# Kernel optimization log

Hardware: AMD Instinct MI355X
Metric: run time of the kernel (lower is better)

The kernel has to match this reference:

```python
import jax, jax.numpy as jnp
import numpy as np

DIM, H, DH = 3072, 24, 128
MLP = int(DIM * 4.0)
EPS = 1e-6


def setup_inputs() -> dict:
    key = jax.random.key(0)
    ks = jax.random.split(key, 8)
    B, L = 2, 4096
    s = 0.02
    return {
        "hidden_states": jax.random.normal(ks[0], (B, L, DIM), jnp.float32),
        "temb": jax.random.normal(ks[1], (B, DIM), jnp.float32),
        "rope": jax.random.normal(ks[2], (L, DH // 2, 4), jnp.float32),
        "w_lin": jax.random.normal(ks[3], (DIM, 3 * DIM), jnp.float32) * s,
        "b_lin": jnp.zeros((3 * DIM,), jnp.float32),
        "w1": jax.random.normal(ks[4], (DIM, 3 * DIM + MLP), jnp.float32) * s,
        "b1": jnp.zeros((3 * DIM + MLP,), jnp.float32),
        "w2": jax.random.normal(ks[5], (DIM + MLP, DIM), jnp.float32) * s,
        "b2": jnp.zeros((DIM,), jnp.float32),
        "q_scale": jnp.ones((DH,), jnp.float32),
        "k_scale": jnp.ones((DH,), jnp.float32),
    }


def _rms(x, scale):
    return x * jax.lax.rsqrt(jnp.mean(x * x, axis=-1, keepdims=True) + EPS) * scale


def _rope(x, fr):
    # x: [B,H,L,DH]; fr: [L, DH//2, 2, 2]
    B, Hn, L, D = x.shape
    x_ = x.reshape(B, Hn, L, D // 2, 1, 2)
    out = fr[..., 0] * x_[..., 0] + fr[..., 1] * x_[..., 1]  # [B,H,L,D//2,2]
    return out.reshape(B, Hn, L, D)


def reference(hidden_states, temb, rope, w_lin, b_lin, w1, b1, w2, b2, q_scale, k_scale):
    B, L, _ = hidden_states.shape
    residual = hidden_states
    # AdaLayerNormZeroSingle
    emb = jax.nn.silu(temb) @ w_lin + b_lin  # [B, 3*DIM]
    shift, scale, gate = jnp.split(emb[:, None, :], 3, axis=-1)
    mu = jnp.mean(hidden_states, axis=-1, keepdims=True)
    var = jnp.mean(jnp.square(hidden_states - mu), axis=-1, keepdims=True)
    x = (hidden_states - mu) * jax.lax.rsqrt(var + EPS)
    x = x * (1 + scale) + shift
    # fused QKV + MLP projection
    proj = x @ w1 + b1
    qkv, mlp = proj[..., : 3 * DIM], proj[..., 3 * DIM :]
    qkv = qkv.reshape(B, L, 3, H, DH).transpose(2, 0, 3, 1, 4)  # [3,B,H,L,DH]
    q, k, v = qkv[0], qkv[1], qkv[2]
    q = _rms(q, q_scale)
    k = _rms(k, k_scale)
    fr = rope.reshape(L, DH // 2, 2, 2)
    q = _rope(q, fr)
    k = _rope(k, fr)
    # heads are MERGED before attention (faithful to source)
    q = q.transpose(0, 2, 1, 3).reshape(B, L, H * DH)
    k = k.transpose(0, 2, 1, 3).reshape(B, L, H * DH)
    v = v.transpose(0, 2, 1, 3).reshape(B, L, H * DH)
    attn = jax.nn.softmax(jnp.einsum("bqd,bkd->bqk", q, k) * (DH ** -0.5), axis=-1)
    attn_out = jnp.einsum("bqk,bkd->bqd", attn, v)
    h = jnp.concatenate([attn_out, jax.nn.gelu(mlp)], axis=-1) @ w2 + b2
    return residual + gate * h
```

## Files before the change

kernel.cpp:

```cpp
#include <hip/hip_runtime.h>
#include <hip/hip_fp16.h>

typedef _Float16 half_t;
typedef __attribute__((ext_vector_type(8))) _Float16 f16x8;
typedef __attribute__((ext_vector_type(4))) float f32x4;

#define DIM   3072
#define NH    24
#define DH    128
#define MLP_D 12288
#define LSEQ  4096
#define BATCH 2
#define NROWS 8192
#define N1    21504
#define QKV_N 9216
#define CAT_N 15360

__device__ __forceinline__ void gload16(const void* g, void* l) {
  __builtin_amdgcn_global_load_lds((const __attribute__((address_space(1))) void*)g,
                                   (__attribute__((address_space(3))) void*)l, 16, 0, 0);
}

__device__ __forceinline__ float gelu_tanh(float x) {
  float u = 0.7978845608028654f * (x + 0.044715f * x * x * x);
  float t = 1.f - 2.f / (__expf(2.f * u) + 1.f);
  return 0.5f * x * (1.f + t);
}

struct EpiParams {
  const float* bias;
  float* outF; int ldoF;
  half_t* o1; int ldo1;
  half_t* o2; int ldo2;
  const float* resid;
  const float* gate;
  float scale;
};

template<int EPI>
__global__ __launch_bounds__(512, 2) void gemm256(
    const half_t* __restrict__ A, int lda,
    const half_t* __restrict__ B, int ldb,
    int nbx, int nper, size_t strA, size_t strB, size_t strO,
    int nsplit, int K, EpiParams ep)
{
  __shared__ __align__(16) char lds[131072];
  const int t = threadIdx.x, lane = t & 63, wid = t >> 6;

  const int nwg = gridDim.x;
  const int wg = blockIdx.x;
  const int id = (wg & 7) * (nwg >> 3) + (wg >> 3);
  const int bz = id / nper;
  const int rid = id - bz * nper;
  const int panel = 8 * nbx;
  const int bm = (rid / panel) * 8 + (rid % 8);
  const int bn = (rid % panel) / 8;
  const int brow = bm * 256, bcol = bn * 256;
  const int wr = wid >> 2, wc = wid & 3;
  A += bz * strA;
  B += bz * strB;

  f32x4 acc[8][4];
#pragma unroll
  for (int m = 0; m < 8; ++m)
#pragma unroll
    for (int n = 0; n < 4; ++n) acc[m][n] = (f32x4){0.f, 0.f, 0.f, 0.f};

  const int scol = (((lane & 3) ^ ((lane >> 3) & 3)) * 8);
  const half_t* pA = A + (size_t)(brow + wid * 32 + (lane >> 2)) * lda + scol;
  const half_t* pB = B + (size_t)(bcol + wid * 32 + (lane >> 2)) * ldb + scol;
  const int wrow = wid * 2048;
  const int NT = K >> 6;

  const int pc = (((lane >> 4) ^ ((lane >> 1) & 3)) << 4);
  const int aoff = (wr * 128 + (lane & 15)) * 64 + pc;
  const int boff = 32768 + (wc * 64 + (lane & 15)) * 64 + pc;

  f16x8 af[2][4], bf[2][4];

#define STAGE_A(bb, kh, tk) {                                               \
    gload16(pA + (size_t)(tk) * 64 + (kh) * 32,                             \
            (bb) + (kh) * 16384 + wrow);                                    \
    gload16(pA + (size_t)(tk) * 64 + (kh) * 32 + (size_t)16 * lda,          \
            (bb) + (kh) * 16384 + wrow + 1024); }
#define STAGE_B(bb, kh, tk) {                                               \
    gload16(pB + (size_t)(tk) * 64 + (kh) * 32,                             \
            (bb) + 32768 + (kh) * 16384 + wrow);                            \
    gload16(pB + (size_t)(tk) * 64 + (kh) * 32 + (size_t)16 * ldb,          \
            (bb) + 32768 + (kh) * 16384 + wrow + 1024); }

#define MFMA_Q(accoff, ab, bb2)                                             \
    _Pragma("unroll")                                                       \
    for (int mi = 0; mi < 4; ++mi)                                          \
      _Pragma("unroll")                                                     \
      for (int nj = 0; nj < 4; ++nj)                                        \
        acc[(accoff) + mi][nj] = __builtin_amdgcn_mfma_f32_16x16x32_f16(    \
            af[ab][mi], bf[bb2][nj], acc[(accoff) + mi][nj], 0, 0, 0);

  {
    char* b0 = lds;
    char* b1 = lds + 65536;
    STAGE_B(b0, 0, 0); STAGE_A(b0, 0, 0); STAGE_B(b0, 1, 0); STAGE_A(b0, 1, 0);
    STAGE_B(b1, 0, 1); STAGE_A(b1, 0, 1); STAGE_B(b1, 1, 1); STAGE_A(b1, 1, 1);
    asm volatile("s_waitcnt vmcnt(8)" ::: "memory");
    __builtin_amdgcn_s_barrier();
#pragma unroll
    for (int mi = 0; mi < 4; ++mi) af[0][mi] = *(const f16x8*)(lds + aoff + mi * 1024);
#pragma unroll
    for (int nj = 0; nj < 4; ++nj) bf[0][nj] = *(const f16x8*)(lds + boff + nj * 1024);
    __builtin_amdgcn_s_barrier();
  }

  for (int tt = 0; tt < NT; ++tt) {
    char* cb = lds + (size_t)(tt & 1) * 65536;
    char* nb = lds + (size_t)((tt & 1) ^ 1) * 65536;

    __builtin_amdgcn_s_setprio(1);
    MFMA_Q(0, 0, 0)
    __builtin_amdgcn_s_setprio(0);
#pragma unroll
    for (int mi = 0; mi < 4; ++mi) af[1][mi] = *(const f16x8*)(cb + aoff + 4096 + mi * 1024);
    if (tt + 2 < NT) STAGE_B(cb, 0, tt + 2);
    __builtin_amdgcn_s_barrier();

    __builtin_amdgcn_s_setprio(1);
    MFMA_Q(4, 1, 0)
    __builtin_amdgcn_s_setprio(0);
#pragma unroll
    for (int mi = 0; mi < 4; ++mi) af[0][mi] = *(const f16x8*)(cb + aoff + 16384 + mi * 1024);
#pragma unroll
    for (int nj = 0; nj < 4; ++nj) bf[1][nj] = *(const f16x8*)(cb + boff + 16384 + nj * 1024);
    if (tt + 2 < NT) STAGE_A(cb, 0, tt + 2);
    __builtin_amdgcn_s_barrier();

    __builtin_amdgcn_s_setprio(1);
    MFMA_Q(0, 0, 1)
    __builtin_amdgcn_s_setprio(0);
#pragma unroll
    for (int mi = 0; mi < 4; ++mi) af[1][mi] = *(const f16x8*)(cb + aoff + 16384 + 4096 + mi * 1024);
    if (tt + 2 < NT) STAGE_B(cb, 1, tt + 2);
    if (tt + 2 < NT) asm volatile("s_waitcnt vmcnt(6)" ::: "memory");
    else             asm volatile("s_waitcnt vmcnt(0)" ::: "memory");
    __builtin_amdgcn_s_barrier();

    __builtin_amdgcn_s_setprio(1);
    MFMA_Q(4, 1, 1)
    __builtin_amdgcn_s_setprio(0);
    if (tt + 1 < NT) {
#pragma unroll
      for (int mi = 0; mi < 4; ++mi) af[0][mi] = *(const f16x8*)(nb + aoff + mi * 1024);
#pragma unroll
      for (int nj = 0; nj < 4; ++nj) bf[0][nj] = *(const f16x8*)(nb + boff + nj * 1024);
    }
    if (tt + 2 < NT) STAGE_A(cb, 1, tt + 2);
    __builtin_amdgcn_s_barrier();
  }
#undef STAGE_A
#undef STAGE_B
#undef MFMA_Q

  half_t* o1 = ep.o1;
  half_t* o2 = ep.o2;
  if (EPI == 1) o1 += (size_t)bz * strO;
  if (EPI == 2) o2 += (size_t)bz * strO;
  const int laneR = lane & 15;
  const int colb = bcol + wc * 64;
  const int rowb = brow + wr * 128 + (lane >> 4) * 4;
#pragma unroll
  for (int mi = 0; mi < 8; ++mi) {
#pragma unroll
    for (int nj = 0; nj < 4; ++nj) {
      int col = colb + nj * 16 + laneR;
#pragma unroll
      for (int j = 0; j < 4; ++j) {
        int row = rowb + mi * 16 + j;
        float v = acc[mi][nj][j];
        if (EPI == 0) {
          v += ep.bias[col];
          if (col < nsplit) {
            o1[(size_t)row * ep.ldo1 + col] = (half_t)v;
          } else {
            o2[(size_t)row * ep.ldo2 + DIM + (col - nsplit)] = (half_t)gelu_tanh(v);
          }
        } else if (EPI == 1) {
          o1[(size_t)row * ep.ldo1 + col] = (half_t)(v * ep.scale);
        } else if (EPI == 2) {
          o2[(size_t)row * ep.ldo2 + col] = (half_t)v;
        } else {
          v += ep.bias[col];
          int b = row >> 12;
          float g = ep.gate[(size_t)b * QKV_N + col];
          float r = ep.resid[(size_t)row * DIM + col];
          ep.outF[(size_t)row * ep.ldoF + col] = r + g * v;
        }
      }
    }
  }
}

__device__ __forceinline__ void tp_tile(
    const float* __restrict__ in, half_t* __restrict__ out, int R, int C,
    int r0, int c0, float (*s)[65], int t)
{
  const int tx = t & 15, ty = t >> 4;
#pragma unroll
  for (int j = 0; j < 4; ++j) {
    int r = ty + j * 16;
    float4 v = *(const float4*)&in[(size_t)(r0 + r) * C + c0 + tx * 4];
    s[r][tx * 4 + 0] = v.x; s[r][tx * 4 + 1] = v.y;
    s[r][tx * 4 + 2] = v.z; s[r][tx * 4 + 3] = v.w;
  }
  __syncthreads();
#pragma unroll
  for (int j = 0; j < 4; ++j) {
    int c = ty + j * 16;
    half_t o[4] = {(half_t)s[tx * 4 + 0][c], (half_t)s[tx * 4 + 1][c],
                   (half_t)s[tx * 4 + 2][c], (half_t)s[tx * 4 + 3][c]};
    *(uint2*)&out[(size_t)(c0 + c) * R + r0 + tx * 4] = *(uint2*)o;
  }
}

#define NBW1 ((N1 / 64) * (DIM / 64))
#define NBW2 ((DIM / 64) * (CAT_N / 64))
#define NBEMB ((QKV_N / 256) * BATCH)

__global__ __launch_bounds__(256) void k_pre(
    const float* __restrict__ w1, half_t* __restrict__ w1T,
    const float* __restrict__ w2, half_t* __restrict__ w2T,
    const float* __restrict__ temb, const float* __restrict__ w_lin,
    const float* __restrict__ b_lin, float* __restrict__ emb)
{
  __shared__ float s[64][65];
  int id = blockIdx.x;
  if (id < NBW1) {
    int cx = id % (N1 / 64), ry = id / (N1 / 64);
    tp_tile(w1, w1T, DIM, N1, ry * 64, cx * 64, s, threadIdx.x);
    return;
  }
  id -= NBW1;
  if (id < NBW2) {
    int cx = id % (DIM / 64), ry = id / (DIM / 64);
    tp_tile(w2, w2T, CAT_N, DIM, ry * 64, cx * 64, s, threadIdx.x);
    return;
  }
  id -= NBW2;
  {
    float* sf = &s[0][0];
    int b = id / (QKV_N / 256);
    int col = (id % (QKV_N / 256)) * 256 + threadIdx.x;
    const float* tr = temb + (size_t)b * DIM;
    for (int k = threadIdx.x; k < DIM; k += 256) {
      float x = tr[k];
      sf[k] = x / (1.f + __expf(-x));
    }
    __syncthreads();
    float acc = b_lin[col];
    for (int k = 0; k < DIM; k += 4) {
      acc += sf[k] * w_lin[(size_t)k * QKV_N + col]
           + sf[k + 1] * w_lin[(size_t)(k + 1) * QKV_N + col]
           + sf[k + 2] * w_lin[(size_t)(k + 2) * QKV_N + col]
           + sf[k + 3] * w_lin[(size_t)(k + 3) * QKV_N + col];
    }
    emb[(size_t)b * QKV_N + col] = acc;
  }
}

__global__ __launch_bounds__(256) void k_lnmod(
    const float* __restrict__ hs, const float* __restrict__ emb,
    half_t* __restrict__ xmod)
{
  int row = blockIdx.x;
  int b = row >> 12;
  const float* x = hs + (size_t)row * DIM;
  int t = threadIdx.x;
  float s = 0.f, s2 = 0.f;
  float4 v[3];
#pragma unroll
  for (int i = 0; i < 3; ++i) {
    v[i] = ((const float4*)x)[t + 256 * i];
    s  += v[i].x + v[i].y + v[i].z + v[i].w;
    s2 += v[i].x * v[i].x + v[i].y * v[i].y + v[i].z * v[i].z + v[i].w * v[i].w;
  }
  for (int o = 32; o; o >>= 1) { s += __shfl_xor(s, o); s2 += __shfl_xor(s2, o); }
  __shared__ float rs[4], rs2[4];
  int lane = t & 63, w = t >> 6;
  if (lane == 0) { rs[w] = s; rs2[w] = s2; }
  __syncthreads();
  s = rs[0] + rs[1] + rs[2] + rs[3];
  s2 = rs2[0] + rs2[1] + rs2[2] + rs2[3];
  float mu = s * (1.f / DIM);
  float var = s2 * (1.f / DIM) - mu * mu;
  float rstd = rsqrtf(var + 1e-6f);
  const float* shift = emb + (size_t)b * QKV_N;
  const float* scale = shift + DIM;
#pragma unroll
  for (int i = 0; i < 3; ++i) {
    int g = t + 256 * i;
    float4 sc = ((const float4*)scale)[g];
    float4 sh = ((const float4*)shift)[g];
    half_t ob[4];
    float vv[4] = {v[i].x, v[i].y, v[i].z, v[i].w};
    float scv[4] = {sc.x, sc.y, sc.z, sc.w};
    float shv[4] = {sh.x, sh.y, sh.z, sh.w};
#pragma unroll
    for (int j = 0; j < 4; ++j) {
      float xn = (vv[j] - mu) * rstd;
      ob[j] = (half_t)(xn * (1.f + scv[j]) + shv[j]);
    }
    *(uint2*)&xmod[(size_t)row * DIM + g * 4] = *(uint2*)ob;
  }
}

#define NROPE ((NROWS * NH * 2) / 4)
#define NVT   ((LSEQ / 64) * (DIM / 64) * BATCH)

__global__ __launch_bounds__(256) void k_ropevt(
    half_t* __restrict__ qkv, const float* __restrict__ rope,
    const float* __restrict__ q_scale, const float* __restrict__ k_scale,
    half_t* __restrict__ vT)
{
  __shared__ half_t s[64][65];
  int id = blockIdx.x;
  if (id < NROPE) {
    int w = id * 4 + (threadIdx.x >> 6);
    int lane = threadIdx.x & 63;
    int qk = w & 1;
    int hr = w >> 1;
    int h = hr % 24;
    int bl = hr / 24;
    size_t base = (size_t)bl * QKV_N + qk * DIM + h * DH;
    float x0 = (float)qkv[base + lane * 2];
    float x1 = (float)qkv[base + lane * 2 + 1];
    float ss = x0 * x0 + x1 * x1;
    for (int o = 32; o; o >>= 1) ss += __shfl_xor(ss, o);
    float r = rsqrtf(ss * (1.f / DH) + 1e-6f);
    const float* sc = qk ? k_scale : q_scale;
    float xs0 = x0 * r * sc[lane * 2];
    float xs1 = x1 * r * sc[lane * 2 + 1];
    int l = bl & (LSEQ - 1);
    float4 fr = ((const float4*)rope)[(size_t)l * 64 + lane];
    qkv[base + lane * 2]     = (half_t)(fr.x * xs0 + fr.y * xs1);
    qkv[base + lane * 2 + 1] = (half_t)(fr.z * xs0 + fr.w * xs1);
    return;
  }
  id -= NROPE;
  {
    int nb = (LSEQ / 64) * (DIM / 64);
    int b = id / nb;
    int rem = id % nb;
    int l0 = (rem % (LSEQ / 64)) * 64, d0 = (rem / (LSEQ / 64)) * 64;
    int tx = threadIdx.x & 63, ty = threadIdx.x >> 6;
#pragma unroll
    for (int j = 0; j < 16; ++j) {
      int l = ty + j * 4;
      s[l][tx] = qkv[(size_t)(b * LSEQ + l0 + l) * QKV_N + 2 * DIM + d0 + tx];
    }
    __syncthreads();
#pragma unroll
    for (int j = 0; j < 16; ++j) {
      int d = ty + j * 4;
      vT[((size_t)b * DIM + d0 + d) * LSEQ + l0 + tx] = s[tx][d];
    }
  }
}

__global__ __launch_bounds__(256) void k_softmax(
    const half_t* __restrict__ S, half_t* __restrict__ P)
{
  int row = blockIdx.x;
  const half_t* srow = S + (size_t)row * LSEQ;
  int t = threadIdx.x;
  f16x8 hv[2];
  float vf[16];
  float mx = -1e30f;
#pragma unroll
  for (int i = 0; i < 2; ++i) {
    hv[i] = ((const f16x8*)srow)[t + 256 * i];
#pragma unroll
    for (int j = 0; j < 8; ++j) {
      vf[i * 8 + j] = (float)hv[i][j];
      mx = fmaxf(mx, vf[i * 8 + j]);
    }
  }
  for (int o = 32; o; o >>= 1) mx = fmaxf(mx, __shfl_xor(mx, o));
  __shared__ float rmx[4], rsum[4];
  int lane = t & 63, w = t >> 6;
  if (lane == 0) rmx[w] = mx;
  __syncthreads();
  mx = fmaxf(fmaxf(rmx[0], rmx[1]), fmaxf(rmx[2], rmx[3]));
  float s = 0.f;
#pragma unroll
  for (int i = 0; i < 16; ++i) {
    vf[i] = __expf(vf[i] - mx);
    s += vf[i];
  }
  for (int o = 32; o; o >>= 1) s += __shfl_xor(s, o);
  if (lane == 0) rsum[w] = s;
  __syncthreads();
  s = rsum[0] + rsum[1] + rsum[2] + rsum[3];
  float inv = 1.f / s;
#pragma unroll
  for (int i = 0; i < 2; ++i) {
    f16x8 ob;
#pragma unroll
    for (int j = 0; j < 8; ++j) ob[j] = (half_t)(vf[i * 8 + j] * inv);
    ((f16x8*)&P[(size_t)row * LSEQ])[t + 256 * i] = ob;
  }
}

__global__ __launch_bounds__(256) void k_final(
    const half_t* __restrict__ part, const float* __restrict__ hs,
    const float* __restrict__ emb, const float* __restrict__ b2,
    float* __restrict__ out)
{
  int row = blockIdx.x;
  int b = row >> 12;
  int t = threadIdx.x;
  const float* gate = emb + (size_t)b * QKV_N + 2 * DIM;
  const half_t* p0 = part + (size_t)row * DIM;
  const half_t* p1 = part + (size_t)NROWS * DIM + (size_t)row * DIM;
  const float* rr = hs + (size_t)row * DIM;
  float* orow = out + (size_t)row * DIM;
#pragma unroll
  for (int i = 0; i < 3; ++i) {
    int g = t + 256 * i;
    short4 a = ((const short4*)p0)[g];
    short4 c = ((const short4*)p1)[g];
    float4 r4 = ((const float4*)rr)[g];
    float4 g4 = ((const float4*)gate)[g];
    float4 b4 = ((const float4*)b2)[g];
    float4 o;
    o.x = r4.x + g4.x * ((float)*(half_t*)&a.x + (float)*(half_t*)&c.x + b4.x);
    o.y = r4.y + g4.y * ((float)*(half_t*)&a.y + (float)*(half_t*)&c.y + b4.y);
    o.z = r4.z + g4.z * ((float)*(half_t*)&a.z + (float)*(half_t*)&c.z + b4.z);
    o.w = r4.w + g4.w * ((float)*(half_t*)&a.w + (float)*(half_t*)&c.w + b4.w);
    ((float4*)orow)[g] = o;
  }
}

extern "C" void kernel_launch(void* const* d_in, const int* in_sizes, int n_in,
                              void* d_out, int out_size, void* d_ws, size_t ws_size,
                              hipStream_t stream) {
  const float* hs      = (const float*)d_in[0];
  const float* temb    = (const float*)d_in[1];
  const float* rope    = (const float*)d_in[2];
  const float* w_lin   = (const float*)d_in[3];
  const float* b_lin   = (const float*)d_in[4];
  const float* w1      = (const float*)d_in[5];
  const float* b1      = (const float*)d_in[6];
  const float* w2      = (const float*)d_in[7];
  const float* b2      = (const float*)d_in[8];
  const float* q_scale = (const float*)d_in[9];
  const float* k_scale = (const float*)d_in[10];
  float* out = (float*)d_out;

  char* ws = (char*)d_ws;
  size_t off = 0;
  auto alloc = [&](size_t bytes) { char* p = ws + off; off += (bytes + 255) & ~(size_t)255; return p; };
  float*  emb    = (float*) alloc((size_t)BATCH * QKV_N * 4);
  half_t* xmod   = (half_t*)alloc((size_t)NROWS * DIM * 2);
  half_t* w1T    = (half_t*)alloc((size_t)N1 * DIM * 2);
  half_t* w2T    = (half_t*)alloc((size_t)DIM * CAT_N * 2);
  half_t* qkv    = (half_t*)alloc((size_t)NROWS * QKV_N * 2);
  half_t* concat = (half_t*)alloc((size_t)NROWS * CAT_N * 2);
  half_t* vT     = (half_t*)alloc((size_t)BATCH * DIM * LSEQ * 2);
  half_t* Sbuf   = (half_t*)alloc((size_t)BATCH * LSEQ * LSEQ * 2);
  half_t* Pbuf   = (half_t*)alloc((size_t)BATCH * LSEQ * LSEQ * 2);
  half_t* part   = xmod;
  (void)ws_size; (void)n_in; (void)in_sizes; (void)out_size;

  k_pre<<<NBW1 + NBW2 + NBEMB, 256, 0, stream>>>(w1, w1T, w2, w2T, temb, w_lin, b_lin, emb);
  k_lnmod<<<NROWS, 256, 0, stream>>>(hs, emb, xmod);

  EpiParams ep1 = {b1, nullptr, 0, qkv, QKV_N, concat, CAT_N, nullptr, nullptr, 0.f};
  gemm256<0><<<(N1 / 256) * (NROWS / 256), 512, 0, stream>>>(
      xmod, DIM, w1T, DIM, N1 / 256, (N1 / 256) * (NROWS / 256), 0, 0, 0, QKV_N, DIM, ep1);

  k_ropevt<<<NROPE + NVT, 256, 0, stream>>>(qkv, rope, q_scale, k_scale, vT);

  EpiParams epS = {nullptr, nullptr, 0, Sbuf, LSEQ, nullptr, 0, nullptr, nullptr, 0.08838834764831845f};
  gemm256<1><<<(LSEQ / 256) * (LSEQ / 256) * BATCH, 512, 0, stream>>>(
      qkv, QKV_N, qkv + DIM, QKV_N,
      LSEQ / 256, (LSEQ / 256) * (LSEQ / 256),
      (size_t)LSEQ * QKV_N, (size_t)LSEQ * QKV_N, (size_t)LSEQ * LSEQ,
      0, DIM, epS);
  k_softmax<<<BATCH * LSEQ, 256, 0, stream>>>(Sbuf, Pbuf);
  EpiParams epPV = {nullptr, nullptr, 0, nullptr, 0, concat, CAT_N, nullptr, nullptr, 0.f};
  gemm256<2><<<(DIM / 256) * (LSEQ / 256) * BATCH, 512, 0, stream>>>(
      Pbuf, LSEQ, vT, LSEQ,
      DIM / 256, (DIM / 256) * (LSEQ / 256),
      (size_t)LSEQ * LSEQ, (size_t)DIM * LSEQ, (size_t)LSEQ * CAT_N,
      0, LSEQ, epPV);

  EpiParams ep2 = {nullptr, nullptr, 0, nullptr, 0, part, DIM, nullptr, nullptr, 0.f};
  gemm256<2><<<(DIM / 256) * (NROWS / 256) * 2, 512, 0, stream>>>(
      concat, CAT_N, w2T, CAT_N,
      DIM / 256, (DIM / 256) * (NROWS / 256),
      (size_t)(CAT_N / 2), (size_t)(CAT_N / 2), (size_t)NROWS * DIM,
      0, CAT_N / 2, ep2);
  k_final<<<NROWS, 256, 0, stream>>>(part, hs, emb, b2, out);
}
```

Measured before the change: 2.624 ms.

## Add 128x256 GEMM kernel with triple-buffered LDS for projection and PV GEMMs

Adds a new gemm128 kernel with 128x256 output tiles, a K-step of 32, a three-slot LDS ring and occupancy hint 4. It replaces gemm256 for the QKV/MLP projection, the PV product and the split-K output projection. gemm256 is kept only for the QK^T score GEMM, so its epilogue is reduced to that one path. Smaller tiles double the workgroup count and allow more concurrent waves per CU to hide latency, at the cost of lower per-tile data reuse and more global traffic.

```diff
diff --git a/kernel.cpp b/kernel.cpp
--- a/kernel.cpp
+++ b/kernel.cpp
@@ -36,6 +36,126 @@
   const float* gate;
   float scale;
 };
+
+template<int EPI>
+__global__ __launch_bounds__(512, 4) void gemm128(
+    const half_t* __restrict__ A, int lda,
+    const half_t* __restrict__ B, int ldb,
+    int nbx, int nper, size_t strA, size_t strB, size_t strO,
+    int nsplit, int K, EpiParams ep)
+{
+  __shared__ __align__(16) char lds[73728];
+  const int t = threadIdx.x, lane = t & 63, wid = t >> 6;
+
+  const int nwg = gridDim.x;
+  const int wg = blockIdx.x;
+  const int id = (wg & 7) * (nwg >> 3) + (wg >> 3);
+  const int bz = id / nper;
+  const int rid = id - bz * nper;
+  const int panel = 8 * nbx;
+  const int bm = (rid / panel) * 8 + (rid % 8);
+  const int bn = (rid % panel) / 8;
+  const int brow = bm * 128, bcol = bn * 256;
+  const int wr = wid >> 2, wc = wid & 3;
+  A += bz * strA;
+  B += bz * strB;
+
+  f32x4 acc[4][4];
+#pragma unroll
+  for (int m = 0; m < 4; ++m)
+#pragma unroll
+    for (int n = 0; n < 4; ++n) acc[m][n] = (f32x4){0.f, 0.f, 0.f, 0.f};
+
+  const int scol = (((lane & 3) ^ ((lane >> 3) & 3)) * 8);
+  const half_t* pA = A + (size_t)(brow + wid * 16 + (lane >> 2)) * lda + scol;
+  const half_t* pB = B + (size_t)(bcol + wid * 32 + (lane >> 2)) * ldb + scol;
+  const int NT = K >> 5;
+
+  const int pc = (((lane >> 4) ^ ((lane >> 1) & 3)) << 4);
+  const int arow  = (wr * 64 + (lane & 15)) * 64 + pc;
+  const int brow_o = 8192 + (wc * 64 + (lane & 15)) * 64 + pc;
+
+  f16x8 af[4], bf[4];
+
+#define STAGE(tk, slot) {                                                   \
+    char* sb = lds + (slot) * 24576;                                        \
+    const half_t* ga = pA + (size_t)(tk) * 32;                              \
+    const half_t* gb = pB + (size_t)(tk) * 32;                              \
+    gload16(ga, sb + wid * 1024);                                           \
+    gload16(gb, sb + 8192 + wid * 2048);                                    \
+    gload16(gb + (size_t)16 * ldb, sb + 8192 + wid * 2048 + 1024); }
+
+#define READF(slot) {                                                       \
+    char* cb = lds + (slot) * 24576;                                        \
+    af[0] = *(const f16x8*)(cb + arow);                                     \
+    af[1] = *(const f16x8*)(cb + arow + 1024);                              \
+    af[2] = *(const f16x8*)(cb + arow + 2048);                              \
+    af[3] = *(const f16x8*)(cb + arow + 3072);                              \
+    bf[0] = *(const f16x8*)(cb + brow_o);                                   \
+    bf[1] = *(const f16x8*)(cb + brow_o + 1024);                            \
+    bf[2] = *(const f16x8*)(cb + brow_o + 2048);                            \
+    bf[3] = *(const f16x8*)(cb + brow_o + 3072); }
+
+  STAGE(0, 0) STAGE(1, 1)
+  asm volatile("s_waitcnt vmcnt(3)" ::: "memory");
+  __builtin_amdgcn_s_barrier();
+  __builtin_amdgcn_sched_barrier(0);
+  READF(0)
+
+  int s0 = 0, s1 = 1, s2 = 2;
+  for (int tt = 0; tt < NT; ++tt) {
+    __builtin_amdgcn_s_setprio(1);
+#pragma unroll
+    for (int mi = 0; mi < 4; ++mi)
+#pragma unroll
+      for (int nj = 0; nj < 4; ++nj)
+        acc[mi][nj] = __builtin_amdgcn_mfma_f32_16x16x32_f16(
+            af[mi], bf[nj], acc[mi][nj], 0, 0, 0);
+    __builtin_amdgcn_s_setprio(0);
+
+    if (tt + 2 < NT) STAGE(tt + 2, s2)
+
+    if (tt + 2 < NT)      asm volatile("s_waitcnt vmcnt(3)" ::: "memory");
+    else if (tt + 1 < NT) asm volatile("s_waitcnt vmcnt(0)" ::: "memory");
+    __builtin_amdgcn_s_barrier();
+    __builtin_amdgcn_sched_barrier(0);
+
+    if (tt + 1 < NT) READF(s1)
+
+    int tmp = s0; s0 = s1; s1 = s2; s2 = tmp;
+  }
+#undef STAGE
+#undef READF
+
+  half_t* o1 = ep.o1;
+  half_t* o2 = ep.o2;
+  if (EPI == 2) o2 += (size_t)bz * strO;
+  const int laneR = lane & 15;
+  const int colb = bcol + wc * 64;
+  const int rowb = brow + wr * 64 + (lane >> 4) * 4;
+#pragma unroll
+  for (int mi = 0; mi < 4; ++mi) {
+#pragma unroll
+    for (int nj = 0; nj < 4; ++nj) {
+      int col = colb + nj * 16 + laneR;
+#pragma unroll
+      for (int j = 0; j < 4; ++j) {
+        int row = rowb + mi * 16 + j;
+        float v = acc[mi][nj][j];
+        if (EPI == 0) {
+          v += ep.bias[col];
+          if (col < nsplit) {
+            o1[(size_t)row * ep.ldo1 + col] = (half_t)v;
+          } else {
+            o2[(size_t)row * ep.ldo2 + DIM + (col - nsplit)] = (half_t)gelu_tanh(v);
+          }
+        } else {
+          o2[(size_t)row * ep.ldo2 + col] = (half_t)v;
+        }
+      }
+    }
+  }
+}
 
 template<int EPI>
 __global__ __launch_bounds__(512, 2) void gemm256(
@@ -160,9 +280,7 @@
 #undef MFMA_Q
 
   half_t* o1 = ep.o1;
-  half_t* o2 = ep.o2;
   if (EPI == 1) o1 += (size_t)bz * strO;
-  if (EPI == 2) o2 += (size_t)bz * strO;
   const int laneR = lane & 15;
   const int colb = bcol + wc * 64;
   const int rowb = brow + wr * 128 + (lane >> 4) * 4;
@@ -175,24 +293,7 @@
       for (int j = 0; j < 4; ++j) {
         int row = rowb + mi * 16 + j;
         float v = acc[mi][nj][j];
-        if (EPI == 0) {
-          v += ep.bias[col];
-          if (col < nsplit) {
-            o1[(size_t)row * ep.ldo1 + col] = (half_t)v;
-          } else {
-            o2[(size_t)row * ep.ldo2 + DIM + (col - nsplit)] = (half_t)gelu_tanh(v);
-          }
-        } else if (EPI == 1) {
-          o1[(size_t)row * ep.ldo1 + col] = (half_t)(v * ep.scale);
-        } else if (EPI == 2) {
-          o2[(size_t)row * ep.ldo2 + col] = (half_t)v;
-        } else {
-          v += ep.bias[col];
-          int b = row >> 12;
-          float g = ep.gate[(size_t)b * QKV_N + col];
-          float r = ep.resid[(size_t)row * DIM + col];
-          ep.outF[(size_t)row * ep.ldoF + col] = r + g * v;
-        }
+        o1[(size_t)row * ep.ldo1 + col] = (half_t)(v * ep.scale);
       }
     }
   }
@@ -473,8 +574,8 @@
   k_lnmod<<<NROWS, 256, 0, stream>>>(hs, emb, xmod);
 
   EpiParams ep1 = {b1, nullptr, 0, qkv, QKV_N, concat, CAT_N, nullptr, nullptr, 0.f};
-  gemm256<0><<<(N1 / 256) * (NROWS / 256), 512, 0, stream>>>(
-      xmod, DIM, w1T, DIM, N1 / 256, (N1 / 256) * (NROWS / 256), 0, 0, 0, QKV_N, DIM, ep1);
+  gemm128<0><<<(N1 / 256) * (NROWS / 128), 512, 0, stream>>>(
+      xmod, DIM, w1T, DIM, N1 / 256, (N1 / 256) * (NROWS / 128), 0, 0, 0, QKV_N, DIM, ep1);
 
   k_ropevt<<<NROPE + NVT, 256, 0, stream>>>(qkv, rope, q_scale, k_scale, vT);
 
@@ -485,17 +586,18 @@
       (size_t)LSEQ * QKV_N, (size_t)LSEQ * QKV_N, (size_t)LSEQ * LSEQ,
       0, DIM, epS);
   k_softmax<<<BATCH * LSEQ, 256, 0, stream>>>(Sbuf, Pbuf);
+
   EpiParams epPV = {nullptr, nullptr, 0, nullptr, 0, concat, CAT_N, nullptr, nullptr, 0.f};
-  gemm256<2><<<(DIM / 256) * (LSEQ / 256) * BATCH, 512, 0, stream>>>(
+  gemm128<2><<<(DIM / 256) * (LSEQ / 128) * BATCH, 512, 0, stream>>>(
       Pbuf, LSEQ, vT, LSEQ,
-      DIM / 256, (DIM / 256) * (LSEQ / 256),
+      DIM / 256, (DIM / 256) * (LSEQ / 128),
       (size_t)LSEQ * LSEQ, (size_t)DIM * LSEQ, (size_t)LSEQ * CAT_N,
       0, LSEQ, epPV);
 
   EpiParams ep2 = {nullptr, nullptr, 0, nullptr, 0, part, DIM, nullptr, nullptr, 0.f};
-  gemm256<2><<<(DIM / 256) * (NROWS / 256) * 2, 512, 0, stream>>>(
+  gemm128<2><<<(DIM / 256) * (NROWS / 128) * 2, 512, 0, stream>>>(
       concat, CAT_N, w2T, CAT_N,
-      DIM / 256, (DIM / 256) * (NROWS / 256),
+      DIM / 256, (DIM / 256) * (NROWS / 128),
       (size_t)(CAT_N / 2), (size_t)(CAT_N / 2), (size_t)NROWS * DIM,
       0, CAT_N / 2, ep2);
   k_final<<<NROWS, 256, 0, stream>>>(part, hs, emb, b2, out);
```

Result: slower. 2.709 ms (+3.2%).

## Split PV GEMM along K into two halves and sum partials

Applied to the files above, without the earlier changes.

The P·V GEMM is split along its K dimension (sequence length) into two halves of 2048. Softmax and the V-transpose kernels now write split-major layouts so each half is a contiguous batch, which doubles the GEMM grid to improve occupancy. A new reduction kernel adds the two fp16 partial results into the concat buffer. The cost is an extra pass over the partial buffer and fp16 rounding of the partials before they are summed.

```diff
diff --git a/kernel.cpp b/kernel.cpp
--- a/kernel.cpp
+++ b/kernel.cpp
@@ -349,6 +349,8 @@
     int b = id / nb;
     int rem = id % nb;
     int l0 = (rem % (LSEQ / 64)) * 64, d0 = (rem / (LSEQ / 64)) * 64;
+    int sl = l0 >> 11;
+    int lof = (l0 & 2047);
     int tx = threadIdx.x & 63, ty = threadIdx.x >> 6;
 #pragma unroll
     for (int j = 0; j < 16; ++j) {
@@ -356,10 +358,11 @@
       s[l][tx] = qkv[(size_t)(b * LSEQ + l0 + l) * QKV_N + 2 * DIM + d0 + tx];
     }
     __syncthreads();
+    half_t* dstb = vT + (size_t)sl * (BATCH * DIM * 2048) + (size_t)b * DIM * 2048;
 #pragma unroll
     for (int j = 0; j < 16; ++j) {
       int d = ty + j * 4;
-      vT[((size_t)b * DIM + d0 + d) * LSEQ + l0 + tx] = s[tx][d];
+      dstb[(size_t)(d0 + d) * 2048 + lof + tx] = s[tx][d];
     }
   }
 }
@@ -404,7 +407,30 @@
     f16x8 ob;
 #pragma unroll
     for (int j = 0; j < 8; ++j) ob[j] = (half_t)(vf[i * 8 + j] * inv);
-    ((f16x8*)&P[(size_t)row * LSEQ])[t + 256 * i] = ob;
+    ((f16x8*)(P + (size_t)i * (BATCH * LSEQ) * 2048 + (size_t)row * 2048))[t] = ob;
+  }
+}
+
+__global__ __launch_bounds__(256) void k_pvsum(
+    const half_t* __restrict__ pv, half_t* __restrict__ concat)
+{
+  int row = blockIdx.x;
+  int b = row >> 12, l = row & (LSEQ - 1);
+  int t = threadIdx.x;
+  const half_t* p0 = pv + ((size_t)(b)     * LSEQ + l) * DIM;
+  const half_t* p1 = pv + ((size_t)(2 + b) * LSEQ + l) * DIM;
+  half_t* dst = concat + (size_t)row * CAT_N;
+#pragma unroll
+  for (int i = 0; i < 3; ++i) {
+    int g = t + 256 * i;
+    short4 a = ((const short4*)p0)[g];
+    short4 c = ((const short4*)p1)[g];
+    half_t o[4];
+    o[0] = (half_t)((float)*(half_t*)&a.x + (float)*(half_t*)&c.x);
+    o[1] = (half_t)((float)*(half_t*)&a.y + (float)*(half_t*)&c.y);
+    o[2] = (half_t)((float)*(half_t*)&a.z + (float)*(half_t*)&c.z);
+    o[3] = (half_t)((float)*(half_t*)&a.w + (float)*(half_t*)&c.w);
+    *(uint2*)&dst[g * 4] = *(uint2*)o;
   }
 }
 
@@ -485,12 +511,14 @@
       (size_t)LSEQ * QKV_N, (size_t)LSEQ * QKV_N, (size_t)LSEQ * LSEQ,
       0, DIM, epS);
   k_softmax<<<BATCH * LSEQ, 256, 0, stream>>>(Sbuf, Pbuf);
-  EpiParams epPV = {nullptr, nullptr, 0, nullptr, 0, concat, CAT_N, nullptr, nullptr, 0.f};
-  gemm256<2><<<(DIM / 256) * (LSEQ / 256) * BATCH, 512, 0, stream>>>(
-      Pbuf, LSEQ, vT, LSEQ,
+
+  EpiParams epPV = {nullptr, nullptr, 0, nullptr, 0, part, DIM, nullptr, nullptr, 0.f};
+  gemm256<2><<<(DIM / 256) * (LSEQ / 256) * 4, 512, 0, stream>>>(
+      Pbuf, 2048, vT, 2048,
       DIM / 256, (DIM / 256) * (LSEQ / 256),
-      (size_t)LSEQ * LSEQ, (size_t)DIM * LSEQ, (size_t)LSEQ * CAT_N,
-      0, LSEQ, epPV);
+      (size_t)LSEQ * 2048, (size_t)DIM * 2048, (size_t)LSEQ * DIM,
+      0, 2048, epPV);
+  k_pvsum<<<NROWS, 256, 0, stream>>>(part, concat);
 
   EpiParams ep2 = {nullptr, nullptr, 0, nullptr, 0, part, DIM, nullptr, nullptr, 0.f};
   gemm256<2><<<(DIM / 256) * (NROWS / 256) * 2, 512, 0, stream>>>(
```

Measured after the change: 2.631 ms. About the same (+0.3%).
